# Optimization experiments

Measured on AMD Instinct MI355X. Metric: run time of the kernel, lower is better.

## Reference

```python
import jax, jax.numpy as jnp
import numpy as np

B, T, I, H = 64, 512, 512, 512

def setup_inputs() -> dict:
    key = jax.random.key(0)
    ks = jax.random.split(key, 13)
    s = 0.02
    return {
        'inputs': jax.random.normal(ks[0], (B, T, I), dtype=jnp.float32),
        'W_i': jax.random.normal(ks[1], (I, H), dtype=jnp.float32) * s,
        'W_f': jax.random.normal(ks[2], (I, H), dtype=jnp.float32) * s,
        'W_o': jax.random.normal(ks[3], (I, H), dtype=jnp.float32) * s,
        'W_c': jax.random.normal(ks[4], (I, H), dtype=jnp.float32) * s,
        'U_i': jax.random.normal(ks[5], (H, H), dtype=jnp.float32) * s,
        'U_f': jax.random.normal(ks[6], (H, H), dtype=jnp.float32) * s,
        'U_o': jax.random.normal(ks[7], (H, H), dtype=jnp.float32) * s,
        'U_c': jax.random.normal(ks[8], (H, H), dtype=jnp.float32) * s,
        'b_i': jax.random.normal(ks[9], (1, H), dtype=jnp.float32) * s,
        'b_f': jax.random.normal(ks[10], (1, H), dtype=jnp.float32) * s,
        'b_o': jax.random.normal(ks[11], (1, H), dtype=jnp.float32) * s,
        'b_c': jax.random.normal(ks[12], (1, H), dtype=jnp.float32) * s,
    }

def reference(inputs, W_i, W_f, W_o, W_c, U_i, U_f, U_o, U_c, b_i, b_f, b_o, b_c):
    batch = inputs.shape[0]
    hidden = U_i.shape[0]
    # Precompute input projections for all 4 gates in one fused GEMM: [T, B, 4H]
    W = jnp.concatenate([W_i, W_f, W_o, W_c], axis=1)          # [I, 4H]
    b = jnp.concatenate([b_i, b_f, b_o, b_c], axis=1)          # [1, 4H]
    U = jnp.concatenate([U_i, U_f, U_o, U_c], axis=1)          # [H, 4H]
    x_proj = jnp.einsum('bti,ig->tbg', inputs, W) + b          # [T, B, 4H]

    def step(carry, xg):
        h, c = carry
        g = xg + h @ U                                          # [B, 4H]
        i_g = jax.nn.sigmoid(g[:, 0*hidden:1*hidden])
        f_g = jax.nn.sigmoid(g[:, 1*hidden:2*hidden])
        o_g = jax.nn.sigmoid(g[:, 2*hidden:3*hidden])
        c_t = jnp.tanh(g[:, 3*hidden:4*hidden])
        c = f_g * c + i_g * c_t
        h = o_g * jnp.tanh(c)
        return (h, c), None

    h0 = jnp.zeros((batch, hidden), dtype=inputs.dtype)
    c0 = jnp.zeros((batch, hidden), dtype=inputs.dtype)
    (h, c), _ = jax.lax.scan(step, (h0, c0), x_proj)
    return h
```

## Files before the change

kernel.cpp:

```cpp
#include <hip/hip_runtime.h>
#include <hip/hip_bf16.h>
#include <cstdint>


typedef __bf16 bf16;
typedef __bf16 bf16x8 __attribute__((ext_vector_type(8)));
typedef float floatx4 __attribute__((ext_vector_type(4)));
typedef uint64_t u64;
typedef uint32_t u32;

#define T_STEPS 512

#define XP_OFF     0ull
#define XBF_OFF    134217728ull
#define WCT_OFF    167772160ull
#define USW_OFF    169869312ull
#define BCAT_OFF   171966464ull
#define HBUF_OFF   171974656ull

__device__ inline u32 pack_bf16x2(float a, float b) {
    union { __bf16 h[2]; u32 u; } cv;
    cv.h[0] = (__bf16)a; cv.h[1] = (__bf16)b;
    return cv.u;
}

__global__ void k0a_convert(const float* __restrict__ in, bf16* __restrict__ xbf) {
    int o = blockIdx.x * 256 + threadIdx.x;
    int k = o & 511;
    int r = o >> 9;
    int t = r >> 6, b = r & 63;
    xbf[o] = (bf16)in[(b * 512 + t) * 512 + k];
}

__global__ void k0b_wcat(const float* __restrict__ Wi, const float* __restrict__ Wf,
                         const float* __restrict__ Wo, const float* __restrict__ Wc,
                         const float* __restrict__ bi, const float* __restrict__ bfv,
                         const float* __restrict__ bo, const float* __restrict__ bc,
                         bf16* __restrict__ wct, float* __restrict__ bcat) {
    int o = blockIdx.x * 256 + threadIdx.x;
    int k = o & 511;
    int c = o >> 9;
    int h = c >> 2, g = c & 3;
    const float* W = (g == 0) ? Wi : (g == 1) ? Wf : (g == 2) ? Wo : Wc;
    wct[o] = (bf16)W[k * 512 + h];
    if (o < 2048) {
        int hh = o >> 2, gg = o & 3;
        const float* bv = (gg == 0) ? bi : (gg == 1) ? bfv : (gg == 2) ? bo : bc;
        bcat[o] = bv[hh];
    }
}

__global__ void k0c_uswz(const float* __restrict__ Ui, const float* __restrict__ Uf,
                         const float* __restrict__ Uo, const float* __restrict__ Uc,
                         bf16* __restrict__ usw) {
    int o = blockIdx.x * 256 + threadIdx.x;
    int e  = o & 7;
    int l  = (o >> 3) & 63;
    int ks = (o >> 9) & 15;
    int nt = (o >> 13) & 1;
    int w  = (o >> 14) & 3;
    int s  = o >> 16;
    int k = ks * 32 + (l >> 4) * 8 + e;
    int col_local = (2 * w + nt) * 16 + (l & 15);
    int h = s * 32 + (col_local >> 2);
    int g = col_local & 3;
    const float* U = (g == 0) ? Ui : (g == 1) ? Uf : (g == 2) ? Uo : Uc;
    usw[o] = (bf16)U[k * 512 + h];
}

__launch_bounds__(256, 2)
__global__ void k1_gemm(const bf16* __restrict__ xbf, const bf16* __restrict__ wct,
                        const float* __restrict__ bcat, bf16* __restrict__ xp) {
    __shared__ bf16 As[128 * 40];
    __shared__ bf16 Bs[128 * 40];
    int tid = threadIdx.x;
    int wid = tid >> 6, lane = tid & 63;
    int q = lane >> 4, m = lane & 15;
    int wr = wid >> 1, wc = wid & 1;
    int br = blockIdx.x & 255, bc = blockIdx.x >> 8;

    floatx4 acc[4][4] = {};

    for (int kk = 0; kk < 16; ++kk) {
        #pragma unroll
        for (int cc = 0; cc < 2; ++cc) {
            int ch = tid + cc * 256;
            int row = ch >> 2, part = ch & 3;
            bf16x8 va = *(const bf16x8*)&xbf[(br * 128 + row) * 512 + kk * 32 + part * 8];
            bf16x8 vb = *(const bf16x8*)&wct[(bc * 128 + row) * 512 + kk * 32 + part * 8];
            *(bf16x8*)&As[row * 40 + part * 8] = va;
            *(bf16x8*)&Bs[row * 40 + part * 8] = vb;
        }
        __syncthreads();
        bf16x8 af[4], bfr[4];
        #pragma unroll
        for (int i = 0; i < 4; ++i) {
            af[i]  = *(const bf16x8*)&As[(wr * 64 + i * 16 + m) * 40 + q * 8];
            bfr[i] = *(const bf16x8*)&Bs[(wc * 64 + i * 16 + m) * 40 + q * 8];
        }
        #pragma unroll
        for (int mt = 0; mt < 4; ++mt)
            #pragma unroll
            for (int nt = 0; nt < 4; ++nt)
                acc[mt][nt] = __builtin_amdgcn_mfma_f32_16x16x32_bf16(
                    af[mt], bfr[nt], acc[mt][nt], 0, 0, 0);
        __syncthreads();
    }
    float bias[4];
    #pragma unroll
    for (int nt = 0; nt < 4; ++nt) bias[nt] = bcat[bc * 128 + wc * 64 + nt * 16 + m];
    #pragma unroll
    for (int mt = 0; mt < 4; ++mt) {
        #pragma unroll
        for (int nt = 0; nt < 4; ++nt) {
            u32 p0 = pack_bf16x2(acc[mt][nt][0] + bias[nt], acc[mt][nt][1] + bias[nt]);
            u32 p1 = pack_bf16x2(acc[mt][nt][2] + bias[nt], acc[mt][nt][3] + bias[nt]);
            size_t idx = (((((size_t)(br * 2 + wr) * 4 + mt) * 16 + bc) * 8
                           + wc * 4 + nt) * 64 + lane) * 4;
            uint2 v; v.x = p0; v.y = p1;
            *(uint2*)&xp[idx] = v;
        }
    }
}

__launch_bounds__(256, 1)
__global__ void k2_rec(const bf16* __restrict__ xp, const bf16* __restrict__ usw,
                       u64* __restrict__ hbuf, float* __restrict__ out) {
    __shared__ bf16 h_lds[16 * 520];
    __shared__ float g_lds[2][128 * 21];
    u32* h32 = (u32*)h_lds;

    int tid = threadIdx.x;
    int wid = tid >> 6, lane = tid & 63;
    int q = lane >> 4, m = lane & 15;
    int bg = blockIdx.x & 3, s = blockIdx.x >> 2;

    bf16x8 bfr[2][16];
    {
        const bf16x8* base = (const bf16x8*)usw;
        #pragma unroll
        for (int nt = 0; nt < 2; ++nt)
            #pragma unroll
            for (int ks = 0; ks < 16; ++ks)
                bfr[nt][ks] = base[(((s * 4 + wid) * 2 + nt) * 16 + ks) * 64 + lane];
    }

    int r = tid >> 4;
    int jc = (tid & 15) * 2;
    float cs0 = 0.f, cs1 = 0.f;

    for (int t = 0; t < T_STEPS; ++t) {
        floatx4 acc[2];
        #pragma unroll
        for (int nt = 0; nt < 2; ++nt) {
            size_t idx = (((((size_t)t * 4 + bg) * 16 + s) * 8 + wid * 2 + nt) * 64 + lane) * 4;
            uint2 v = *(const uint2*)&xp[idx];
            acc[nt][0] = __builtin_bit_cast(float, v.x << 16);
            acc[nt][1] = __builtin_bit_cast(float, v.x & 0xffff0000u);
            acc[nt][2] = __builtin_bit_cast(float, v.y << 16);
            acc[nt][3] = __builtin_bit_cast(float, v.y & 0xffff0000u);
        }

        if (t > 0) {
            const u64* rb = hbuf + ((size_t)((t - 1) & 1) * 4 + bg) * 4096;
            u32 tg = (u32)t;
            u64 w[16];
            #pragma unroll
            for (int i = 0; i < 16; ++i)
                w[i] = __hip_atomic_load(rb + tid + 256 * i, __ATOMIC_RELAXED,
                                         __HIP_MEMORY_SCOPE_AGENT);
            while (true) {
                bool ok = true;
                #pragma unroll
                for (int i = 0; i < 16; ++i) ok &= ((u32)(w[i] >> 32) == tg);
                if (ok) break;
                #pragma unroll
                for (int i = 0; i < 16; ++i)
                    w[i] = __hip_atomic_load(rb + tid + 256 * i, __ATOMIC_RELAXED,
                                             __HIP_MEMORY_SCOPE_AGENT);
            }
            #pragma unroll
            for (int i = 0; i < 16; ++i)
                h32[i * 260 + tid] = (u32)w[i];
            __syncthreads();
            #pragma unroll
            for (int ks = 0; ks < 16; ++ks) {
                bf16x8 a = *(const bf16x8*)&h_lds[m * 520 + ks * 32 + q * 8];
                acc[0] = __builtin_amdgcn_mfma_f32_16x16x32_bf16(a, bfr[0][ks], acc[0], 0, 0, 0);
                acc[1] = __builtin_amdgcn_mfma_f32_16x16x32_bf16(a, bfr[1][ks], acc[1], 0, 0, 0);
            }
        }

        float* gl = g_lds[t & 1];
        #pragma unroll
        for (int nt = 0; nt < 2; ++nt) {
            int col = (2 * wid + nt) * 16 + m;
            *(floatx4*)&gl[col * 21 + q * 4] = acc[nt];
        }
        __syncthreads();

        float h0, h1;
        {
            float gi = gl[(jc * 4 + 0) * 21 + r];
            float gf = gl[(jc * 4 + 1) * 21 + r];
            float go = gl[(jc * 4 + 2) * 21 + r];
            float gc = gl[(jc * 4 + 3) * 21 + r];
            float ig = 1.f / (1.f + __expf(-gi));
            float fg = 1.f / (1.f + __expf(-gf));
            float og = 1.f / (1.f + __expf(-go));
            float th = 1.f - 2.f / (__expf(2.f * gc) + 1.f);
            cs0 = fg * cs0 + ig * th;
            h0 = og * (1.f - 2.f / (__expf(2.f * cs0) + 1.f));
        }
        {
            float gi = gl[((jc + 1) * 4 + 0) * 21 + r];
            float gf = gl[((jc + 1) * 4 + 1) * 21 + r];
            float go = gl[((jc + 1) * 4 + 2) * 21 + r];
            float gc = gl[((jc + 1) * 4 + 3) * 21 + r];
            float ig = 1.f / (1.f + __expf(-gi));
            float fg = 1.f / (1.f + __expf(-gf));
            float og = 1.f / (1.f + __expf(-go));
            float th = 1.f - 2.f / (__expf(2.f * gc) + 1.f);
            cs1 = fg * cs1 + ig * th;
            h1 = og * (1.f - 2.f / (__expf(2.f * cs1) + 1.f));
        }
        u64 word = ((u64)(u32)(t + 1) << 32) | (u64)pack_bf16x2(h0, h1);
        __hip_atomic_store(hbuf + (((size_t)(t & 1) * 4 + bg) * 16 + r) * 256
                                + s * 16 + (tid & 15),
                           word, __ATOMIC_RELAXED, __HIP_MEMORY_SCOPE_AGENT);
        if (t == T_STEPS - 1) {
            out[(bg * 16 + r) * 512 + s * 32 + jc]     = h0;
            out[(bg * 16 + r) * 512 + s * 32 + jc + 1] = h1;
        }
    }
}

extern "C" void kernel_launch(void* const* d_in, const int* in_sizes, int n_in,
                              void* d_out, int out_size, void* d_ws, size_t ws_size,
                              hipStream_t stream) {
    const float* inp = (const float*)d_in[0];
    const float* Wi  = (const float*)d_in[1];
    const float* Wf  = (const float*)d_in[2];
    const float* Wo  = (const float*)d_in[3];
    const float* Wc  = (const float*)d_in[4];
    const float* Ui  = (const float*)d_in[5];
    const float* Uf  = (const float*)d_in[6];
    const float* Uo  = (const float*)d_in[7];
    const float* Uc  = (const float*)d_in[8];
    const float* bi  = (const float*)d_in[9];
    const float* bfv = (const float*)d_in[10];
    const float* bo  = (const float*)d_in[11];
    const float* bc  = (const float*)d_in[12];

    char* ws = (char*)d_ws;
    bf16*  xp    = (bf16*)(ws + XP_OFF);
    bf16*  xbf   = (bf16*)(ws + XBF_OFF);
    bf16*  wct   = (bf16*)(ws + WCT_OFF);
    bf16*  usw   = (bf16*)(ws + USW_OFF);
    float* bcat  = (float*)(ws + BCAT_OFF);
    u64*   hbuf  = (u64*)(ws + HBUF_OFF);

    k0a_convert<<<65536, 256, 0, stream>>>(inp, xbf);
    k0b_wcat<<<4096, 256, 0, stream>>>(Wi, Wf, Wo, Wc, bi, bfv, bo, bc, wct, bcat);
    k0c_uswz<<<4096, 256, 0, stream>>>(Ui, Uf, Uo, Uc, usw);
    k1_gemm<<<4096, 256, 0, stream>>>(xbf, wct, bcat, xp);
    k2_rec<<<64, 256, 0, stream>>>(xp, usw, hbuf, (float*)d_out);
}
```

Before: 1.456 ms.

## Replace LDS gate transpose and barrier with in-register shuffles in recurrent step

After: 1.723 ms. 1.18x slower.

```diff
diff --git a/kernel.cpp b/kernel.cpp
--- a/kernel.cpp
+++ b/kernel.cpp
@@ -23,6 +23,8 @@
     cv.h[0] = (__bf16)a; cv.h[1] = (__bf16)b;
     return cv.u;
 }
+__device__ inline float bf_lo(u32 w) { return __builtin_bit_cast(float, w << 16); }
+__device__ inline float bf_hi(u32 w) { return __builtin_bit_cast(float, w & 0xffff0000u); }
 
 __global__ void k0a_convert(const float* __restrict__ in, bf16* __restrict__ xbf) {
     int o = blockIdx.x * 256 + threadIdx.x;
@@ -126,13 +128,13 @@
 __launch_bounds__(256, 1)
 __global__ void k2_rec(const bf16* __restrict__ xp, const bf16* __restrict__ usw,
                        u64* __restrict__ hbuf, float* __restrict__ out) {
-    __shared__ bf16 h_lds[16 * 520];
-    __shared__ float g_lds[2][128 * 21];
+    __shared__ bf16 h_lds[16 * 544];
     u32* h32 = (u32*)h_lds;
 
     int tid = threadIdx.x;
     int wid = tid >> 6, lane = tid & 63;
     int q = lane >> 4, m = lane & 15;
+    int v = m >> 2, a = m & 3;
     int bg = blockIdx.x & 3, s = blockIdx.x >> 2;
 
     bf16x8 bfr[2][16];
@@ -145,21 +147,21 @@
                 bfr[nt][ks] = base[(((s * 4 + wid) * 2 + nt) * 16 + ks) * 64 + lane];
     }
 
-    int r = tid >> 4;
-    int jc = (tid & 15) * 2;
+    int ra = q * 4 + a;
     float cs0 = 0.f, cs1 = 0.f;
+    int pc_local = 4 * wid + 2 * (v & 1) + (v >> 1);
+    int u0 = 8 * wid + v, u1 = 8 * wid + 4 + v;
 
     for (int t = 0; t < T_STEPS; ++t) {
-        floatx4 acc[2];
-        #pragma unroll
-        for (int nt = 0; nt < 2; ++nt) {
-            size_t idx = (((((size_t)t * 4 + bg) * 16 + s) * 8 + wid * 2 + nt) * 64 + lane) * 4;
-            uint2 v = *(const uint2*)&xp[idx];
-            acc[nt][0] = __builtin_bit_cast(float, v.x << 16);
-            acc[nt][1] = __builtin_bit_cast(float, v.x & 0xffff0000u);
-            acc[nt][2] = __builtin_bit_cast(float, v.y << 16);
-            acc[nt][3] = __builtin_bit_cast(float, v.y & 0xffff0000u);
-        }
+        uint2 vx0, vx1;
+        {
+            size_t b0 = (((((size_t)t * 4 + bg) * 16 + s) * 8 + wid * 2 + 0) * 64 + lane) * 4;
+            size_t b1 = (((((size_t)t * 4 + bg) * 16 + s) * 8 + wid * 2 + 1) * 64 + lane) * 4;
+            vx0 = *(const uint2*)&xp[b0];
+            vx1 = *(const uint2*)&xp[b1];
+        }
+
+        floatx4 acc[2] = {};
 
         if (t > 0) {
             const u64* rb = hbuf + ((size_t)((t - 1) & 1) * 4 + bg) * 4096;
@@ -181,56 +183,64 @@
             }
             #pragma unroll
             for (int i = 0; i < 16; ++i)
-                h32[i * 260 + tid] = (u32)w[i];
+                h32[i * 272 + tid] = (u32)w[i];
             __syncthreads();
             #pragma unroll
             for (int ks = 0; ks < 16; ++ks) {
-                bf16x8 a = *(const bf16x8*)&h_lds[m * 520 + ks * 32 + q * 8];
-                acc[0] = __builtin_amdgcn_mfma_f32_16x16x32_bf16(a, bfr[0][ks], acc[0], 0, 0, 0);
-                acc[1] = __builtin_amdgcn_mfma_f32_16x16x32_bf16(a, bfr[1][ks], acc[1], 0, 0, 0);
-            }
-        }
-
-        float* gl = g_lds[t & 1];
+                bf16x8 af = *(const bf16x8*)&h_lds[m * 544 + ks * 32 + q * 8];
+                acc[0] = __builtin_amdgcn_mfma_f32_16x16x32_bf16(af, bfr[0][ks], acc[0], 0, 0, 0);
+                acc[1] = __builtin_amdgcn_mfma_f32_16x16x32_bf16(af, bfr[1][ks], acc[1], 0, 0, 0);
+            }
+        }
+
+        acc[0][0] += bf_lo(vx0.x); acc[0][1] += bf_hi(vx0.x);
+        acc[0][2] += bf_lo(vx0.y); acc[0][3] += bf_hi(vx0.y);
+        acc[1][0] += bf_lo(vx1.x); acc[1][1] += bf_hi(vx1.x);
+        acc[1][2] += bf_lo(vx1.y); acc[1][3] += bf_hi(vx1.y);
+
+        float h0, h1;
         #pragma unroll
         for (int nt = 0; nt < 2; ++nt) {
-            int col = (2 * wid + nt) * 16 + m;
-            *(floatx4*)&gl[col * 21 + q * 4] = acc[nt];
-        }
-        __syncthreads();
-
-        float h0, h1;
-        {
-            float gi = gl[(jc * 4 + 0) * 21 + r];
-            float gf = gl[(jc * 4 + 1) * 21 + r];
-            float go = gl[(jc * 4 + 2) * 21 + r];
-            float gc = gl[(jc * 4 + 3) * 21 + r];
-            float ig = 1.f / (1.f + __expf(-gi));
-            float fg = 1.f / (1.f + __expf(-gf));
-            float og = 1.f / (1.f + __expf(-go));
-            float th = 1.f - 2.f / (__expf(2.f * gc) + 1.f);
-            cs0 = fg * cs0 + ig * th;
-            h0 = og * (1.f - 2.f / (__expf(2.f * cs0) + 1.f));
-        }
-        {
-            float gi = gl[((jc + 1) * 4 + 0) * 21 + r];
-            float gf = gl[((jc + 1) * 4 + 1) * 21 + r];
-            float go = gl[((jc + 1) * 4 + 2) * 21 + r];
-            float gc = gl[((jc + 1) * 4 + 3) * 21 + r];
-            float ig = 1.f / (1.f + __expf(-gi));
-            float fg = 1.f / (1.f + __expf(-gf));
-            float og = 1.f / (1.f + __expf(-go));
-            float th = 1.f - 2.f / (__expf(2.f * gc) + 1.f);
-            cs1 = fg * cs1 + ig * th;
-            h1 = og * (1.f - 2.f / (__expf(2.f * cs1) + 1.f));
-        }
-        u64 word = ((u64)(u32)(t + 1) << 32) | (u64)pack_bf16x2(h0, h1);
-        __hip_atomic_store(hbuf + (((size_t)(t & 1) * 4 + bg) * 16 + r) * 256
-                                + s * 16 + (tid & 15),
+            float x0 = acc[nt][0], x1 = acc[nt][1], x2 = acc[nt][2], x3 = acc[nt][3];
+            {
+                int a0 = a & 1;
+                float p0 = a0 ? x0 : x1;
+                float p1 = a0 ? x2 : x3;
+                float r0 = __shfl_xor(p0, 1, 64);
+                float r1 = __shfl_xor(p1, 1, 64);
+                x0 = a0 ? r0 : x0;  x1 = a0 ? x1 : r0;
+                x2 = a0 ? r1 : x2;  x3 = a0 ? x3 : r1;
+            }
+            {
+                int a1 = (a >> 1) & 1;
+                float p0 = a1 ? x0 : x2;
+                float p1 = a1 ? x1 : x3;
+                float r0 = __shfl_xor(p0, 2, 64);
+                float r1 = __shfl_xor(p1, 2, 64);
+                x0 = a1 ? r0 : x0;  x2 = a1 ? x2 : r0;
+                x1 = a1 ? r1 : x1;  x3 = a1 ? x3 : r1;
+            }
+            float ig = 1.f / (1.f + __expf(-x0));
+            float fg = 1.f / (1.f + __expf(-x1));
+            float og = 1.f / (1.f + __expf(-x2));
+            float th = 1.f - 2.f / (__expf(2.f * x3) + 1.f);
+            float& cs = nt ? cs1 : cs0;
+            cs = fg * cs + ig * th;
+            float hv = og * (1.f - 2.f / (__expf(2.f * cs) + 1.f));
+            if (nt) h1 = hv; else h0 = hv;
+        }
+
+        float hx0 = __shfl_xor(h0, 4, 64);
+        float hx1 = __shfl_xor(h1, 4, 64);
+        float he = (v & 1) ? hx1 : h0;
+        float ho = (v & 1) ? h1  : hx0;
+        u64 word = ((u64)(u32)(t + 1) << 32) | (u64)pack_bf16x2(he, ho);
+        __hip_atomic_store(hbuf + ((((size_t)(t & 1) * 4 + bg) * 16 + ra) * 256)
+                                + s * 16 + pc_local,
                            word, __ATOMIC_RELAXED, __HIP_MEMORY_SCOPE_AGENT);
         if (t == T_STEPS - 1) {
-            out[(bg * 16 + r) * 512 + s * 32 + jc]     = h0;
-            out[(bg * 16 + r) * 512 + s * 32 + jc + 1] = h1;
+            out[(bg * 16 + ra) * 512 + s * 32 + u0] = h0;
+            out[(bg * 16 + ra) * 512 + s * 32 + u1] = h1;
         }
     }
 }
```
